# Kernel optimization log

Hardware: AMD Instinct MI355X
Metric: run time of the kernel (lower is better)

## Reference

```python
import jax, jax.numpy as jnp
import numpy as np

# Llama-2-7B-like config with GQA
T, D, N, K, H = 2048, 4096, 32, 8, 128
THETA = 10000.0


def _rope(x, positions):
    """Split-ordering RoPE on last dim H of x: [..., T, heads, H]."""
    half = H // 2
    inv_freq = 1.0 / (THETA ** (jnp.arange(half, dtype=jnp.float32) / half))  # theta^(-2i/H)
    ang = positions.astype(jnp.float32)[:, None] * inv_freq[None, :]          # [T, half]
    cos = jnp.cos(ang)[:, None, :]
    sin = jnp.sin(ang)[:, None, :]
    x1, x2 = x[..., :half], x[..., half:]
    return jnp.concatenate([x1 * cos - x2 * sin, x2 * cos + x1 * sin], axis=-1).astype(x.dtype)


def setup_inputs() -> dict:
    key = jax.random.key(0)
    ks = jax.random.split(key, 5)
    s_in = 1.0 / np.sqrt(D)
    s_out = 1.0 / np.sqrt(N * H)
    return {
        "x": jax.random.normal(ks[0], (T, D), jnp.float32),
        "positions": jnp.arange(T, dtype=jnp.int32),
        "w_q": jax.random.normal(ks[1], (D, N, H), jnp.float32) * s_in,
        "w_k": jax.random.normal(ks[2], (D, K, H), jnp.float32) * s_in,
        "w_v": jax.random.normal(ks[3], (D, K, H), jnp.float32) * s_in,
        "w_o": jax.random.normal(ks[4], (N, H, D), jnp.float32) * s_out,
    }


def reference(x, positions, w_q, w_k, w_v, w_o):
    """Prefill path: fused QKV proj + RoPE + causal GQA attention + o_proj."""
    G = N // K  # query heads per kv head
    q = jnp.einsum('td,dnh->tnh', x, w_q)
    k = jnp.einsum('sd,dkh->skh', x, w_k)
    v = jnp.einsum('sd,dkh->skh', x, w_v)
    q = _rope(q, positions)
    k = _rope(k, positions)
    qg = q.reshape(T, K, G, H)
    scores = jnp.einsum('tkgh,skh->kgts', qg, k) * (H ** -0.5)
    causal = positions[:, None] >= positions[None, :]  # [T, S]
    scores = jnp.where(causal[None, None], scores, jnp.finfo(scores.dtype).min)
    probs = jax.nn.softmax(scores, axis=-1)
    out = jnp.einsum('kgts,skh->tkgh', probs, v).reshape(T, N, H)
    return jnp.einsum('tnh,nhd->td', out, w_o)
```

## Files before the change

kernel.cpp:

```cpp
#include <hip/hip_runtime.h>
#include <hip/hip_bf16.h>
#include <math.h>

#define T_SEQ   2048
#define D_MODEL 4096
#define N_Q     32
#define N_KV    8
#define HDIM    128
#define NH      (N_Q * HDIM)
#define KH      (N_KV * HDIM)
#define QKV_W   (NH + 2 * KH)

using bf16   = __hip_bfloat16;
using short8 = __attribute__((ext_vector_type(8))) short;
using floatx4 = __attribute__((ext_vector_type(4))) float;

__device__ __forceinline__ void load_lds16(const bf16* g, bf16* l) {
  __builtin_amdgcn_global_load_lds((const __attribute__((address_space(1))) void*)g,
                                   (__attribute__((address_space(3))) void*)l,
                                   16, 0, 0);
}

__global__ void cvt_bf16_kernel(const float* __restrict__ src, bf16* __restrict__ dst, int n4) {
  int i = blockIdx.x * 256 + threadIdx.x;
  if (i < n4) {
    const float4 v = ((const float4*)src)[i];
    union { bf16 h[4]; unsigned long long u; } o;
    o.h[0] = __float2bfloat16(v.x); o.h[1] = __float2bfloat16(v.y);
    o.h[2] = __float2bfloat16(v.z); o.h[3] = __float2bfloat16(v.w);
    ((unsigned long long*)dst)[i] = o.u;
  }
}

__global__ void sincos_tab(const int* __restrict__ pos, float* __restrict__ ct,
                           float* __restrict__ st) {
  const int i = blockIdx.x * 256 + threadIdx.x;
  const int t = i >> 6, h = i & 63;
  const float p = (float)pos[t];
  const float inv = exp2f(-(float)h * 0.20762050592420985f);
  float s, c; sincosf(p * inv, &s, &c);
  ct[i] = c; st[i] = s;
}

__global__ __launch_bounds__(256)
void transpose_cvt(const float* __restrict__ src, bf16* __restrict__ dst, int R, int C) {
  __shared__ float tile[64][65];
  const int bx = blockIdx.x * 64;
  const int by = blockIdx.y * 64;
  const int c4 = (threadIdx.x & 15) * 4;
  const int r0 = threadIdx.x >> 4;
#pragma unroll
  for (int i = 0; i < 4; i++) {
    const float4 v = *(const float4*)&src[(size_t)(by + r0 + i * 16) * C + bx + c4];
    tile[r0 + i * 16][c4 + 0] = v.x;
    tile[r0 + i * 16][c4 + 1] = v.y;
    tile[r0 + i * 16][c4 + 2] = v.z;
    tile[r0 + i * 16][c4 + 3] = v.w;
  }
  __syncthreads();
  const int cc = threadIdx.x >> 2;
  const int rq = (threadIdx.x & 3) * 16;
  union { bf16 h[8]; short8 s; } o0, o1;
#pragma unroll
  for (int j = 0; j < 8; j++) {
    o0.h[j] = __float2bfloat16(tile[rq + j][cc]);
    o1.h[j] = __float2bfloat16(tile[rq + 8 + j][cc]);
  }
  bf16* d = dst + (size_t)(bx + cc) * R + by + rq;
  *(short8*)(d)     = o0.s;
  *(short8*)(d + 8) = o1.s;
}

#define A_SLOT 16384
#define B_SLOT 8192
#define B_BASE (3 * A_SLOT)
template <int EPI>
__global__ __launch_bounds__(512, 2)
void gemm_p3(const bf16* __restrict__ A, const bf16* __restrict__ B,
             float* __restrict__ Cf, int N, int Kc,
             const float* __restrict__ cosT, const float* __restrict__ sinT,
             bf16* __restrict__ Qo, bf16* __restrict__ Ko, bf16* __restrict__ Vo) {
  __shared__ __align__(16) bf16 smem[3 * A_SLOT + 2 * B_SLOT];
  const int tid  = threadIdx.x;
  const int lane = tid & 63;
  const int w    = tid >> 6;
  const int bm = blockIdx.x * 256;
  const int bn = blockIdx.y * 128;
  const int wr = w >> 1;
  const int wc = w & 1;
  const int r = lane & 15, q = lane >> 4;

  const int rl = lane >> 3, ch = lane & 7;
  const int swz = (ch ^ (rl & 7)) * 8;
  const bf16* gA = A + (size_t)(bm + w * 32 + rl) * Kc + swz;
  const bf16* gB = B + (size_t)(bn + w * 16 + rl) * Kc + swz;
  const int ldsA0 = w * 32 * 64;
  const int ldsB0 = w * 16 * 64;

  floatx4 acc[4][4];
  const floatx4 zero = {0.f, 0.f, 0.f, 0.f};
#pragma unroll
  for (int i = 0; i < 4; i++)
#pragma unroll
    for (int j = 0; j < 4; j++) acc[i][j] = zero;

#pragma unroll
  for (int t = 0; t < 2; t++) {
#pragma unroll
    for (int i = 0; i < 4; i++)
      load_lds16(gA + t * 64 + (size_t)i * 8 * Kc, smem + t * A_SLOT + ldsA0 + i * 8 * 64);
#pragma unroll
    for (int j = 0; j < 2; j++)
      load_lds16(gB + t * 64 + (size_t)j * 8 * Kc, smem + B_BASE + t * B_SLOT + ldsB0 + j * 8 * 64);
  }

#define RD_A(H)                                                                 \
  _Pragma("unroll") for (int m2 = 0; m2 < 2; m2++)                              \
  _Pragma("unroll") for (int ks = 0; ks < 2; ks++)                              \
    aT[H][m2][ks] = *(const short8*)(As + (wr * 64 + (H) * 32 + m2 * 16 + r) * 64 \
                                        + (((ks * 4 + q) ^ (r & 7)) * 8));
#define RD_B(H)                                                                 \
  _Pragma("unroll") for (int n2 = 0; n2 < 2; n2++)                              \
  _Pragma("unroll") for (int ks = 0; ks < 2; ks++)                              \
    bT[H][n2][ks] = *(const short8*)(Bs + (wc * 64 + (H) * 32 + n2 * 16 + r) * 64 \
                                        + (((ks * 4 + q) ^ (r & 7)) * 8));
#define MM(MQ, NQ)                                                              \
  __builtin_amdgcn_s_setprio(1);                                                \
  _Pragma("unroll") for (int ks = 0; ks < 2; ks++)                              \
  _Pragma("unroll") for (int m2 = 0; m2 < 2; m2++)                              \
  _Pragma("unroll") for (int n2 = 0; n2 < 2; n2++)                              \
    acc[(MQ)*2+m2][(NQ)*2+n2] = __builtin_amdgcn_mfma_f32_16x16x32_bf16(        \
        aT[MQ][m2][ks], bT[NQ][n2][ks], acc[(MQ)*2+m2][(NQ)*2+n2], 0, 0, 0);    \
  __builtin_amdgcn_s_setprio(0);
#define ST_A(i) load_lds16(gA + kA + (size_t)(i) * 8 * Kc, SdA + (i) * 8 * 64)
#define ST_B(j) load_lds16(gB + kB + (size_t)(j) * 8 * Kc, SdB + (j) * 8 * 64)

  const int NT = Kc >> 6;
  int a_ring = 0;
  for (int g = 0; g < NT; ++g) {
    if (g == 0)          asm volatile("s_waitcnt vmcnt(6)" ::: "memory");
    else if (g + 1 < NT) asm volatile("s_waitcnt vmcnt(4)" ::: "memory");
    else                 asm volatile("s_waitcnt vmcnt(0)" ::: "memory");
    __builtin_amdgcn_s_barrier();

    const bf16* As = smem + a_ring * A_SLOT;
    const bf16* Bs = smem + B_BASE + (g & 1) * B_SLOT;
    int sa = a_ring - 1; if (sa < 0) sa = 2;
    bf16* SdA = smem + sa * A_SLOT + ldsA0;
    bf16* SdB = smem + B_BASE + ((g + 1) & 1) * B_SLOT + ldsB0;
    const bool stA = (g + 2 < NT);
    const bool stB = (g >= 1) && (g + 1 < NT);
    const int kA = (g + 2) * 64, kB = (g + 1) * 64;

    short8 aT[2][2][2], bT[2][2][2];
    RD_A(0); RD_B(0);
    if (stB) { ST_B(0); ST_B(1); }
    __builtin_amdgcn_s_barrier();
    MM(0, 0);
    __builtin_amdgcn_s_barrier();
    RD_B(1);
    if (stA) { ST_A(0); ST_A(1); }
    __builtin_amdgcn_s_barrier();
    MM(0, 1);
    __builtin_amdgcn_s_barrier();
    RD_A(1);
    if (stA) { ST_A(2); }
    __builtin_amdgcn_s_barrier();
    MM(1, 1);
    __builtin_amdgcn_s_barrier();
    if (stA) { ST_A(3); }
    MM(1, 0);

    a_ring = (a_ring + 1 == 3) ? 0 : a_ring + 1;
  }
#undef RD_A
#undef RD_B
#undef MM
#undef ST_A
#undef ST_B

  if (EPI == 1) {
#pragma unroll
    for (int mt = 0; mt < 4; mt++)
#pragma unroll
      for (int nt = 0; nt < 4; nt++)
#pragma unroll
        for (int reg = 0; reg < 4; reg++) {
          const int row = bm + wr * 64 + mt * 16 + q * 4 + reg;
          const int col = bn + wc * 64 + nt * 16 + r;
          Cf[(size_t)row * N + col] = acc[mt][nt][reg];
        }
  } else {
    __syncthreads();
#pragma unroll
    for (int mt = 0; mt < 4; mt++)
#pragma unroll
      for (int nt = 0; nt < 4; nt++)
#pragma unroll
        for (int reg = 0; reg < 4; reg++)
          smem[(wr * 64 + mt * 16 + q * 4 + reg) * 137 + wc * 64 + nt * 16 + r] =
              __float2bfloat16(acc[mt][nt][reg]);
    __syncthreads();

    const int hn = blockIdx.y;
    if (hn < N_Q + N_KV) {
      const float SCL = 0.12751744868673310f;
      const bool isQ = (hn < N_Q);
      bf16* base = isQ ? (Qo + (size_t)bm * NH + hn * HDIM)
                       : (Ko + (size_t)bm * KH + (hn - N_Q) * HDIM);
      const int ostride = isQ ? NH : KH;
      for (int idx = tid; idx < 256 * 64; idx += 512) {
        const int row = idx >> 6, h = idx & 63;
        const float x1 = __bfloat162float(smem[row * 137 + h]);
        const float x2 = __bfloat162float(smem[row * 137 + h + 64]);
        const float cs = cosT[(bm + row) * 64 + h];
        const float sn = sinT[(bm + row) * 64 + h];
        float o1 = x1 * cs - x2 * sn;
        float o2 = x2 * cs + x1 * sn;
        if (isQ) { o1 *= SCL; o2 *= SCL; }
        bf16* d = base + (size_t)row * ostride;
        d[h]      = __float2bfloat16(o1);
        d[h + 64] = __float2bfloat16(o2);
      }
    } else {
      const int kh = hn - (N_Q + N_KV);
      for (int idx = tid; idx < 128 * 64; idx += 512) {
        const int h = idx >> 6, r4 = (idx & 63) * 4;
        union { bf16 h4[4]; unsigned long long u; } o;
#pragma unroll
        for (int j = 0; j < 4; j++) o.h4[j] = smem[(r4 + j) * 137 + h];
        *(unsigned long long*)(Vo + ((size_t)kh * HDIM + h) * T_SEQ + bm + r4) = o.u;
      }
    }
  }
}

#define MSHIFT 8.0f
__global__ __launch_bounds__(256, 2)
void flash_attn(const bf16* __restrict__ Q, const bf16* __restrict__ Kk,
                const bf16* __restrict__ Vt, bf16* __restrict__ O) {
  const int id = blockIdx.x;
  const int n  = id & 31;
  const int kh = n >> 2;
  const int bt = (id < 256) ? (15 - (id >> 5)) : ((id - 256) >> 5);
  const int t0 = bt * 128;
  const int tid = threadIdx.x, lane = tid & 63, w = tid >> 6;
  const int r = lane & 15, q = lane >> 4;

  __shared__ bf16 Ks[64][128];
  __shared__ bf16 Vs[128][64];
  __shared__ bf16 Ps[4][32][72];

  short8 qf[2][4];
#pragma unroll
  for (int mf = 0; mf < 2; mf++) {
    const bf16* qrow = Q + (size_t)(t0 + w * 32 + mf * 16 + r) * NH + n * HDIM;
#pragma unroll
    for (int ks = 0; ks < 4; ks++)
      qf[mf][ks] = *(const short8*)(qrow + ks * 32 + q * 8);
  }

  floatx4 o_acc[2][8];
  const floatx4 zero = {0.f, 0.f, 0.f, 0.f};
#pragma unroll
  for (int mf = 0; mf < 2; mf++)
#pragma unroll
    for (int i = 0; i < 8; i++) o_acc[mf][i] = zero;
  float l_lane[2][4];
#pragma unroll
  for (int mf = 0; mf < 2; mf++)
#pragma unroll
    for (int i = 0; i < 4; i++) l_lane[mf][i] = 0.f;

  const int krl = lane >> 4, kc = lane & 15;
  const int vrl = lane >> 3, vc = lane & 7;

  const int nIter = 2 * bt + 2;
  for (int it = 0; it < nIter; ++it) {
    const int s0 = it * 64;
    __syncthreads();
#pragma unroll
    for (int i = 0; i < 4; i++) {
      const int row = (w * 4 + i) * 4 + krl;
      load_lds16(Kk + (size_t)(s0 + row) * KH + kh * HDIM + (kc ^ (row & 7)) * 8,
                 &Ks[(w * 4 + i) * 4][0]);
    }
#pragma unroll
    for (int i = 0; i < 4; i++) {
      const int row = (w * 4 + i) * 8 + vrl;
      load_lds16(Vt + ((size_t)kh * HDIM + row) * T_SEQ + s0 + (vc ^ (row & 7)) * 8,
                 &Vs[(w * 4 + i) * 8][0]);
    }
    __syncthreads();

    floatx4 sa[2][4];
#pragma unroll
    for (int mf = 0; mf < 2; mf++)
#pragma unroll
      for (int nt = 0; nt < 4; nt++) sa[mf][nt] = zero;
#pragma unroll
    for (int ks = 0; ks < 4; ks++)
#pragma unroll
      for (int nt = 0; nt < 4; nt++) {
        const int krow = nt * 16 + r;
        const short8 kb = *(const short8*)(&Ks[krow][(((ks * 4 + q) ^ (krow & 7))) * 8]);
#pragma unroll
        for (int mf = 0; mf < 2; mf++)
          sa[mf][nt] = __builtin_amdgcn_mfma_f32_16x16x32_bf16(qf[mf][ks], kb, sa[mf][nt], 0, 0, 0);
      }

#pragma unroll
    for (int mf = 0; mf < 2; mf++) {
      const int rbase = t0 + w * 32 + mf * 16;
      if (s0 + 63 > rbase) {
#pragma unroll
        for (int nt = 0; nt < 4; nt++)
#pragma unroll
          for (int reg = 0; reg < 4; reg++) {
            const int trow = rbase + q * 4 + reg;
            const int scol = s0 + nt * 16 + r;
            if (scol > trow) sa[mf][nt][reg] = -INFINITY;
          }
      }
#pragma unroll
      for (int nt = 0; nt < 4; nt++)
#pragma unroll
        for (int reg = 0; reg < 4; reg++) {
          const float p = exp2f(sa[mf][nt][reg] - MSHIFT);
          l_lane[mf][reg] += p;
          Ps[w][mf * 16 + q * 4 + reg][nt * 16 + r] = __float2bfloat16(p);
        }
    }

    __asm__ volatile("s_waitcnt lgkmcnt(0)" ::: "memory");

#pragma unroll
    for (int ks = 0; ks < 2; ks++) {
      short8 pa[2];
#pragma unroll
      for (int mf = 0; mf < 2; mf++)
        pa[mf] = *(const short8*)(&Ps[w][mf * 16 + r][ks * 32 + q * 8]);
#pragma unroll
      for (int ht = 0; ht < 8; ht++) {
        const int vrow = ht * 16 + r;
        const short8 vb = *(const short8*)(&Vs[vrow][(((ks * 4 + q) ^ (vrow & 7))) * 8]);
#pragma unroll
        for (int mf = 0; mf < 2; mf++)
          o_acc[mf][ht] = __builtin_amdgcn_mfma_f32_16x16x32_bf16(pa[mf], vb, o_acc[mf][ht], 0, 0, 0);
      }
    }
  }

#pragma unroll
  for (int mf = 0; mf < 2; mf++)
#pragma unroll
    for (int reg = 0; reg < 4; reg++) {
      float v = l_lane[mf][reg];
      v += __shfl_xor(v, 1); v += __shfl_xor(v, 2);
      v += __shfl_xor(v, 4); v += __shfl_xor(v, 8);
      const float inv_l = 1.0f / v;
      const int trow = t0 + w * 32 + mf * 16 + q * 4 + reg;
#pragma unroll
      for (int ht = 0; ht < 8; ht++)
        O[(size_t)trow * NH + n * HDIM + ht * 16 + r] =
            __float2bfloat16(o_acc[mf][ht][reg] * inv_l);
    }
}

extern "C" void kernel_launch(void* const* d_in, const int* in_sizes, int n_in,
                              void* d_out, int out_size, void* d_ws, size_t ws_size,
                              hipStream_t stream) {
  (void)in_sizes; (void)n_in; (void)out_size; (void)ws_size;
  const float* x   = (const float*)d_in[0];
  const int* pos   = (const int*)d_in[1];
  const float* w_q = (const float*)d_in[2];
  const float* w_k = (const float*)d_in[3];
  const float* w_v = (const float*)d_in[4];
  const float* w_o = (const float*)d_in[5];
  float* out = (float*)d_out;

  char* ws = (char*)d_ws;
  bf16*  xb   = (bf16*)(ws);
  bf16*  Bq   = (bf16*)(ws + (16ULL << 20));
  bf16*  Qr   = (bf16*)(ws + (64ULL << 20));
  bf16*  Kr   = (bf16*)(ws + (80ULL << 20));
  bf16*  Vt   = (bf16*)(ws + (84ULL << 20));
  bf16*  Oatt = (bf16*)(ws + (88ULL << 20));
  float* ct   = (float*)(ws + (104ULL << 20));
  float* st   = (float*)(ws + (105ULL << 20));
  bf16*  woT  = Bq;

  cvt_bf16_kernel<<<(T_SEQ * D_MODEL / 4 + 255) / 256, 256, 0, stream>>>(x, xb, T_SEQ * D_MODEL / 4);
  sincos_tab<<<(T_SEQ * 64) / 256, 256, 0, stream>>>(pos, ct, st);
  transpose_cvt<<<dim3(NH / 64, D_MODEL / 64), 256, 0, stream>>>(w_q, Bq, D_MODEL, NH);
  transpose_cvt<<<dim3(KH / 64, D_MODEL / 64), 256, 0, stream>>>(w_k, Bq + (size_t)NH * D_MODEL, D_MODEL, KH);
  transpose_cvt<<<dim3(KH / 64, D_MODEL / 64), 256, 0, stream>>>(w_v, Bq + (size_t)(NH + KH) * D_MODEL, D_MODEL, KH);

  gemm_p3<2><<<dim3(T_SEQ / 256, QKV_W / 128), 512, 0, stream>>>(
      xb, Bq, nullptr, QKV_W, D_MODEL, ct, st, Qr, Kr, Vt);

  transpose_cvt<<<dim3(D_MODEL / 64, NH / 64), 256, 0, stream>>>(w_o, woT, NH, D_MODEL);

  flash_attn<<<dim3(512), 256, 0, stream>>>(Qr, Kr, Vt, Oatt);

  gemm_p3<1><<<dim3(T_SEQ / 256, D_MODEL / 128), 512, 0, stream>>>(
      Oatt, woT, out, D_MODEL, NH, nullptr, nullptr, nullptr, nullptr, nullptr);
}
```

Baseline: 510.0 us.

## Restructure GEMM inner loop to k-slice order with fewer barriers

The GEMM main loop no longer splits each 64-wide K tile into four quadrant phases with a barrier between each. It now reads all A/B fragments for the first k-slice, issues every global-to-LDS prefetch for the next stages at once, takes one barrier, then reads the second k-slice and runs 16 MFMAs per slice. The goal is to cut per-iteration barrier and synchronisation overhead and give the compiler larger independent MFMA batches. In exchange it loses the fine-grained interleaving of LDS reads, prefetches and MFMAs, and holds more fragment registers live at once.

```diff
diff --git a/kernel.cpp b/kernel.cpp
--- a/kernel.cpp
+++ b/kernel.cpp
@@ -114,23 +114,19 @@
       load_lds16(gB + t * 64 + (size_t)j * 8 * Kc, smem + B_BASE + t * B_SLOT + ldsB0 + j * 8 * 64);
   }
 
-#define RD_A(H)                                                                 \
-  _Pragma("unroll") for (int m2 = 0; m2 < 2; m2++)                              \
-  _Pragma("unroll") for (int ks = 0; ks < 2; ks++)                              \
-    aT[H][m2][ks] = *(const short8*)(As + (wr * 64 + (H) * 32 + m2 * 16 + r) * 64 \
-                                        + (((ks * 4 + q) ^ (r & 7)) * 8));
-#define RD_B(H)                                                                 \
-  _Pragma("unroll") for (int n2 = 0; n2 < 2; n2++)                              \
-  _Pragma("unroll") for (int ks = 0; ks < 2; ks++)                              \
-    bT[H][n2][ks] = *(const short8*)(Bs + (wc * 64 + (H) * 32 + n2 * 16 + r) * 64 \
-                                        + (((ks * 4 + q) ^ (r & 7)) * 8));
-#define MM(MQ, NQ)                                                              \
+#define RD_KS(KS)                                                               \
+  _Pragma("unroll") for (int mt = 0; mt < 4; mt++)                              \
+    aT[mt][KS] = *(const short8*)(As + (wr * 64 + mt * 16 + r) * 64             \
+                                     + ((((KS) * 4 + q) ^ (r & 7)) * 8));       \
+  _Pragma("unroll") for (int nt = 0; nt < 4; nt++)                              \
+    bT[nt][KS] = *(const short8*)(Bs + (wc * 64 + nt * 16 + r) * 64             \
+                                     + ((((KS) * 4 + q) ^ (r & 7)) * 8));
+#define MM_KS(KS)                                                               \
   __builtin_amdgcn_s_setprio(1);                                                \
-  _Pragma("unroll") for (int ks = 0; ks < 2; ks++)                              \
-  _Pragma("unroll") for (int m2 = 0; m2 < 2; m2++)                              \
-  _Pragma("unroll") for (int n2 = 0; n2 < 2; n2++)                              \
-    acc[(MQ)*2+m2][(NQ)*2+n2] = __builtin_amdgcn_mfma_f32_16x16x32_bf16(        \
-        aT[MQ][m2][ks], bT[NQ][n2][ks], acc[(MQ)*2+m2][(NQ)*2+n2], 0, 0, 0);    \
+  _Pragma("unroll") for (int mt = 0; mt < 4; mt++)                              \
+  _Pragma("unroll") for (int nt = 0; nt < 4; nt++)                              \
+    acc[mt][nt] = __builtin_amdgcn_mfma_f32_16x16x32_bf16(                      \
+        aT[mt][KS], bT[nt][KS], acc[mt][nt], 0, 0, 0);                          \
   __builtin_amdgcn_s_setprio(0);
 #define ST_A(i) load_lds16(gA + kA + (size_t)(i) * 8 * Kc, SdA + (i) * 8 * 64)
 #define ST_B(j) load_lds16(gB + kB + (size_t)(j) * 8 * Kc, SdB + (j) * 8 * 64)
@@ -152,30 +148,20 @@
     const bool stB = (g >= 1) && (g + 1 < NT);
     const int kA = (g + 2) * 64, kB = (g + 1) * 64;
 
-    short8 aT[2][2][2], bT[2][2][2];
-    RD_A(0); RD_B(0);
+    short8 aT[4][2], bT[4][2];
+    RD_KS(0);
     if (stB) { ST_B(0); ST_B(1); }
+    if (stA) { ST_A(0); ST_A(1); ST_A(2); ST_A(3); }
     __builtin_amdgcn_s_barrier();
-    MM(0, 0);
-    __builtin_amdgcn_s_barrier();
-    RD_B(1);
-    if (stA) { ST_A(0); ST_A(1); }
-    __builtin_amdgcn_s_barrier();
-    MM(0, 1);
-    __builtin_amdgcn_s_barrier();
-    RD_A(1);
-    if (stA) { ST_A(2); }
-    __builtin_amdgcn_s_barrier();
-    MM(1, 1);
-    __builtin_amdgcn_s_barrier();
-    if (stA) { ST_A(3); }
-    MM(1, 0);
+
+    RD_KS(1);
+    MM_KS(0);
+    MM_KS(1);
 
     a_ring = (a_ring + 1 == 3) ? 0 : a_ring + 1;
   }
-#undef RD_A
-#undef RD_B
-#undef MM
+#undef RD_KS
+#undef MM_KS
 #undef ST_A
 #undef ST_B
 
```

Result: no change. 517.7 us (+1.5%).
